# Kernel optimization log

Measured on AMD Instinct MI355X. Metric: run time of the kernel, lower is better.

## Reference

```python
import jax, jax.numpy as jnp
import numpy as np

MARGIN = 0.2
N_CLASSES = 100
BETA_INIT = 1.2
EPS = 1e-8


def setup_inputs() -> dict:
    key = jax.random.key(0)
    k1, k2, k3 = jax.random.split(key, 3)
    BS, DIM, T = 4096, 128, 500000
    batch = jax.random.normal(k1, (BS, DIM), dtype=jnp.float32)
    labels = jax.random.randint(k2, (BS,), 0, N_CLASSES, dtype=jnp.int64)
    triplets = jax.random.randint(k3, (T, 3), 0, BS, dtype=jnp.int64)
    beta = jnp.ones((N_CLASSES,), dtype=jnp.float32) * BETA_INIT
    return {"batch": batch, "labels": labels, "triplets": triplets, "beta": beta}


def reference(batch, labels, triplets, beta):
    # Gather anchor/positive/negative embedding rows: [T, DIM]
    a = batch[triplets[:, 0]]
    p = batch[triplets[:, 1]]
    n = batch[triplets[:, 2]]
    # Euclidean distances with the module's 1e-8 stabilizer: [T]
    d_ap = jnp.sqrt(jnp.sum((a - p) ** 2, axis=-1) + EPS)
    d_an = jnp.sqrt(jnp.sum((a - n) ** 2, axis=-1) + EPS)
    # Learned per-class beta, indexed by the anchor's label: [T]
    b = beta[labels[triplets[:, 0]]]
    pos_loss = jax.nn.relu(d_ap - b + MARGIN)
    neg_loss = jax.nn.relu(b - d_an + MARGIN)
    pair_count = (jnp.sum((pos_loss > 0.0).astype(jnp.float32))
                  + jnp.sum((neg_loss > 0.0).astype(jnp.float32)))
    total = jnp.sum(pos_loss + neg_loss)
    # If no active pairs, torch code returns the (zero) unnormalized sum.
    return jnp.where(pair_count > 0.0, total / jnp.maximum(pair_count, 1.0), total)
```

## Files before the change

### kernel.cpp

```cpp
#include <hip/hip_runtime.h>

#define MARGIN 0.2f
#define EPS 1e-8f
#define GRID_BLOCKS 2048

__global__ __launch_bounds__(256) void triplet_loss_kernel(
    const float* __restrict__ batch,
    const int* __restrict__ labels,
    const int* __restrict__ triplets,
    const float* __restrict__ beta,
    float* __restrict__ partial,
    int T)
{
    const int lane = threadIdx.x & 63;
    const int wid  = threadIdx.x >> 6;
    const int sub  = lane >> 3;
    const int fi   = lane & 7;

    float loss = 0.f, cnt = 0.f;

    for (int base = blockIdx.x * 32; base < T; base += gridDim.x * 32) {
        int t = base + wid * 8 + sub;
        if (t < T) {
            int ai = triplets[3 * t + 0];
            int pi = triplets[3 * t + 1];
            int ni = triplets[3 * t + 2];
            float b = beta[labels[ai]];
            const float4* __restrict__ arow = (const float4*)(batch + ((size_t)ai << 7));
            const float4* __restrict__ prow = (const float4*)(batch + ((size_t)pi << 7));
            const float4* __restrict__ nrow = (const float4*)(batch + ((size_t)ni << 7));
            float sap = 0.f, san = 0.f;
            #pragma unroll
            for (int k = 0; k < 4; ++k) {
                float4 av = arow[fi + 8 * k];
                float4 pv = prow[fi + 8 * k];
                float4 nv = nrow[fi + 8 * k];
                float d;
                d = av.x - pv.x; sap += d * d;
                d = av.y - pv.y; sap += d * d;
                d = av.z - pv.z; sap += d * d;
                d = av.w - pv.w; sap += d * d;
                d = av.x - nv.x; san += d * d;
                d = av.y - nv.y; san += d * d;
                d = av.z - nv.z; san += d * d;
                d = av.w - nv.w; san += d * d;
            }
            #pragma unroll
            for (int off = 4; off >= 1; off >>= 1) {
                sap += __shfl_xor(sap, off);
                san += __shfl_xor(san, off);
            }
            float d_ap = sqrtf(sap + EPS);
            float d_an = sqrtf(san + EPS);
            float pos = fmaxf(d_ap - b + MARGIN, 0.f);
            float neg = fmaxf(b - d_an + MARGIN, 0.f);
            loss += pos + neg;
            cnt  += (pos > 0.f ? 1.f : 0.f) + (neg > 0.f ? 1.f : 0.f);
        }
    }

    #pragma unroll
    for (int off = 32; off >= 1; off >>= 1) {
        loss += __shfl_down(loss, off);
        cnt  += __shfl_down(cnt, off);
    }
    __shared__ float sl[4], sc[4];
    if (lane == 0) { sl[wid] = loss; sc[wid] = cnt; }
    __syncthreads();
    if (threadIdx.x == 0) {
        partial[blockIdx.x * 2 + 0] = sl[0] + sl[1] + sl[2] + sl[3];
        partial[blockIdx.x * 2 + 1] = sc[0] + sc[1] + sc[2] + sc[3];
    }
}

__global__ __launch_bounds__(1024) void triplet_finalize_kernel(
    const float* __restrict__ partial, float* __restrict__ out, int nblocks)
{
    float L = 0.f, C = 0.f;
    for (int i = threadIdx.x; i < nblocks; i += blockDim.x) {
        L += partial[2 * i + 0];
        C += partial[2 * i + 1];
    }
    #pragma unroll
    for (int off = 32; off >= 1; off >>= 1) {
        L += __shfl_down(L, off);
        C += __shfl_down(C, off);
    }
    __shared__ float sl[16], sc[16];
    int wid  = threadIdx.x >> 6;
    int lane = threadIdx.x & 63;
    int nw   = blockDim.x >> 6;
    if (lane == 0) { sl[wid] = L; sc[wid] = C; }
    __syncthreads();
    if (threadIdx.x == 0) {
        float Lt = 0.f, Ct = 0.f;
        for (int i = 0; i < nw; ++i) { Lt += sl[i]; Ct += sc[i]; }
        Lt *= 0.125f;
        Ct *= 0.125f;
        out[0] = (Ct > 0.f) ? (Lt / fmaxf(Ct, 1.f)) : Lt;
    }
}

extern "C" void kernel_launch(void* const* d_in, const int* in_sizes, int n_in,
                              void* d_out, int out_size, void* d_ws, size_t ws_size,
                              hipStream_t stream) {
    const float* batch    = (const float*)d_in[0];
    const int*   labels   = (const int*)d_in[1];
    const int*   triplets = (const int*)d_in[2];
    const float* beta     = (const float*)d_in[3];
    float* out     = (float*)d_out;
    float* partial = (float*)d_ws;

    int T = in_sizes[2] / 3;
    int grid = GRID_BLOCKS;
    int groups = (T + 31) / 32;
    if (grid > groups) grid = groups;

    triplet_loss_kernel<<<grid, 256, 0, stream>>>(batch, labels, triplets, beta, partial, T);
    triplet_finalize_kernel<<<1, 1024, 0, stream>>>(partial, out, grid);
}
```

Measured before the change: 37.42 us.

## Convert embeddings to fp16 and compute distances with packed fdot2

Adds a pre-pass that converts the batch embeddings to fp16 in the workspace, then gathers fp16 rows (half the bytes per triplet) and accumulates squared differences with packed fdot2 into fp32. Each triplet is now handled by 4 lanes instead of 8, so a block covers 64 triplets per step, and the finalize scale is adjusted to match. The intent is to cut gather traffic and ALU work. The cost is an extra conversion launch and reduced precision on the differences, which could shift results near the relu thresholds.

```diff
diff --git a/kernel.cpp b/kernel.cpp
--- a/kernel.cpp
+++ b/kernel.cpp
@@ -4,7 +4,95 @@
 #define EPS 1e-8f
 #define GRID_BLOCKS 2048
 
-__global__ __launch_bounds__(256) void triplet_loss_kernel(
+typedef _Float16 h2 __attribute__((ext_vector_type(2)));
+typedef _Float16 h8 __attribute__((ext_vector_type(8)));
+union H8 { h8 v; h2 p[4]; };
+
+
+__global__ __launch_bounds__(256) void convert_f32_to_f16_kernel(
+    const float* __restrict__ in, _Float16* __restrict__ out, int n4)
+{
+    int i = blockIdx.x * blockDim.x + threadIdx.x;
+    if (i < n4) {
+        float4 f = *(const float4*)(in + 4 * (size_t)i);
+        h2 lo, hi;
+        lo.x = (_Float16)f.x; lo.y = (_Float16)f.y;
+        hi.x = (_Float16)f.z; hi.y = (_Float16)f.w;
+        *(h2*)(out + 4 * (size_t)i)     = lo;
+        *(h2*)(out + 4 * (size_t)i + 2) = hi;
+    }
+}
+
+__global__ __launch_bounds__(256) void triplet_loss_f16_kernel(
+    const _Float16* __restrict__ batch16,
+    const int* __restrict__ labels,
+    const int* __restrict__ triplets,
+    const float* __restrict__ beta,
+    float* __restrict__ partial,
+    int T)
+{
+    const int lane = threadIdx.x & 63;
+    const int wid  = threadIdx.x >> 6;
+    const int sub  = lane >> 2;
+    const int fi   = lane & 3;
+
+    float loss = 0.f, cnt = 0.f;
+
+    for (int base = blockIdx.x * 64; base < T; base += gridDim.x * 64) {
+        int t = base + wid * 16 + sub;
+        if (t < T) {
+            int ai = triplets[3 * t + 0];
+            int pi = triplets[3 * t + 1];
+            int ni = triplets[3 * t + 2];
+            float b = beta[labels[ai]];
+            const h8* __restrict__ arow = (const h8*)(batch16 + ((size_t)ai << 7));
+            const h8* __restrict__ prow = (const h8*)(batch16 + ((size_t)pi << 7));
+            const h8* __restrict__ nrow = (const h8*)(batch16 + ((size_t)ni << 7));
+            float sap = 0.f, san = 0.f;
+            #pragma unroll
+            for (int k = 0; k < 4; ++k) {
+                H8 a, p, n, dp, dn;
+                a.v = arow[fi + 4 * k];
+                p.v = prow[fi + 4 * k];
+                n.v = nrow[fi + 4 * k];
+                dp.v = a.v - p.v;
+                dn.v = a.v - n.v;
+                #pragma unroll
+                for (int j = 0; j < 4; ++j) {
+                    sap = __builtin_amdgcn_fdot2(dp.p[j], dp.p[j], sap, false);
+                    san = __builtin_amdgcn_fdot2(dn.p[j], dn.p[j], san, false);
+                }
+            }
+            #pragma unroll
+            for (int off = 2; off >= 1; off >>= 1) {
+                sap += __shfl_xor(sap, off);
+                san += __shfl_xor(san, off);
+            }
+            float d_ap = sqrtf(sap + EPS);
+            float d_an = sqrtf(san + EPS);
+            float pos = fmaxf(d_ap - b + MARGIN, 0.f);
+            float neg = fmaxf(b - d_an + MARGIN, 0.f);
+            loss += pos + neg;
+            cnt  += (pos > 0.f ? 1.f : 0.f) + (neg > 0.f ? 1.f : 0.f);
+        }
+    }
+
+    #pragma unroll
+    for (int off = 32; off >= 1; off >>= 1) {
+        loss += __shfl_down(loss, off);
+        cnt  += __shfl_down(cnt, off);
+    }
+    __shared__ float sl[4], sc[4];
+    if (lane == 0) { sl[wid] = loss; sc[wid] = cnt; }
+    __syncthreads();
+    if (threadIdx.x == 0) {
+        partial[blockIdx.x * 2 + 0] = sl[0] + sl[1] + sl[2] + sl[3];
+        partial[blockIdx.x * 2 + 1] = sc[0] + sc[1] + sc[2] + sc[3];
+    }
+}
+
+
+__global__ __launch_bounds__(256) void triplet_loss_f32_kernel(
     const float* __restrict__ batch,
     const int* __restrict__ labels,
     const int* __restrict__ triplets,
@@ -73,8 +161,10 @@
     }
 }
 
+
 __global__ __launch_bounds__(1024) void triplet_finalize_kernel(
-    const float* __restrict__ partial, float* __restrict__ out, int nblocks)
+    const float* __restrict__ partial, float* __restrict__ out, int nblocks,
+    float scale)
 {
     float L = 0.f, C = 0.f;
     for (int i = threadIdx.x; i < nblocks; i += blockDim.x) {
@@ -95,8 +185,8 @@
     if (threadIdx.x == 0) {
         float Lt = 0.f, Ct = 0.f;
         for (int i = 0; i < nw; ++i) { Lt += sl[i]; Ct += sc[i]; }
-        Lt *= 0.125f;
-        Ct *= 0.125f;
+        Lt *= scale;
+        Ct *= scale;
         out[0] = (Ct > 0.f) ? (Lt / fmaxf(Ct, 1.f)) : Lt;
     }
 }
@@ -108,14 +198,32 @@
     const int*   labels   = (const int*)d_in[1];
     const int*   triplets = (const int*)d_in[2];
     const float* beta     = (const float*)d_in[3];
-    float* out     = (float*)d_out;
-    float* partial = (float*)d_ws;
-
+    float* out = (float*)d_out;
+
+    int nbatch = in_sizes[0];
     int T = in_sizes[2] / 3;
-    int grid = GRID_BLOCKS;
-    int groups = (T + 31) / 32;
-    if (grid > groups) grid = groups;
-
-    triplet_loss_kernel<<<grid, 256, 0, stream>>>(batch, labels, triplets, beta, partial, T);
-    triplet_finalize_kernel<<<1, 1024, 0, stream>>>(partial, out, grid);
-}
+
+    size_t f16_bytes = (size_t)nbatch * sizeof(_Float16);
+    size_t need = f16_bytes + (size_t)GRID_BLOCKS * 2 * sizeof(float);
+
+    if (ws_size >= need) {
+        _Float16* batch16 = (_Float16*)d_ws;
+        float* partial = (float*)((char*)d_ws + f16_bytes);
+
+        int n4 = nbatch / 4;
+        convert_f32_to_f16_kernel<<<(n4 + 255) / 256, 256, 0, stream>>>(batch, batch16, n4);
+
+        int grid = GRID_BLOCKS;
+        int groups = (T + 63) / 64;
+        if (grid > groups) grid = groups;
+        triplet_loss_f16_kernel<<<grid, 256, 0, stream>>>(batch16, labels, triplets, beta, partial, T);
+        triplet_finalize_kernel<<<1, 1024, 0, stream>>>(partial, out, grid, 0.25f);
+    } else {
+        float* partial = (float*)d_ws;
+        int grid = GRID_BLOCKS;
+        int groups = (T + 31) / 32;
+        if (grid > groups) grid = groups;
+        triplet_loss_f32_kernel<<<grid, 256, 0, stream>>>(batch, labels, triplets, beta, partial, T);
+        triplet_finalize_kernel<<<1, 1024, 0, stream>>>(partial, out, grid, 0.125f);
+    }
+}
```

Result: faster. 30.97 us (-17.2%).

## Replace per-triplet row gathers with bf16 MFMA Gram matrix lookup

Applied to the files above, without the earlier changes.

Distances are rewritten as ||a||^2+||b||^2-2a·b. The new path precomputes row norms and a full 4096x4096 Gram matrix with bf16 MFMA, stored as fp16. Each triplet then does two scalar lookups into that matrix instead of gathering three 512-byte rows, which removes most of the per-triplet gather traffic. The cost is writing and randomly reading a 32MB matrix, extra launches, and reduced precision from bf16 inputs, fp16 storage and cancellation in the norm expansion. An fp32 fallback runs if the workspace is too small.

```diff
diff --git a/kernel.cpp b/kernel.cpp
--- a/kernel.cpp
+++ b/kernel.cpp
@@ -1,10 +1,171 @@
 #include <hip/hip_runtime.h>
+#include <hip/hip_fp16.h>
 
 #define MARGIN 0.2f
 #define EPS 1e-8f
-#define GRID_BLOCKS 2048
-
-__global__ __launch_bounds__(256) void triplet_loss_kernel(
+
+typedef short bf16x8 __attribute__((ext_vector_type(8)));
+typedef float f32x4 __attribute__((ext_vector_type(4)));
+
+static __device__ __forceinline__ unsigned short f32_to_bf16(float x) {
+    unsigned v = __float_as_uint(x);
+    unsigned r = (v + 0x7FFFu + ((v >> 16) & 1u)) >> 16;
+    return (unsigned short)r;
+}
+
+__global__ __launch_bounds__(256) void prep_norms_kernel(
+    const float* __restrict__ batch,
+    unsigned short* __restrict__ xb,
+    float* __restrict__ norms,
+    int rows)
+{
+    int gid = blockIdx.x * blockDim.x + threadIdx.x;
+    int r = gid >> 4, c = (gid & 15) * 8;
+    if (r >= rows) return;
+    const float4* src = (const float4*)(batch + (size_t)r * 128 + c);
+    float4 f0 = src[0], f1 = src[1];
+    float s = f0.x*f0.x + f0.y*f0.y + f0.z*f0.z + f0.w*f0.w
+            + f1.x*f1.x + f1.y*f1.y + f1.z*f1.z + f1.w*f1.w;
+    ushort4 u0, u1;
+    u0.x = f32_to_bf16(f0.x); u0.y = f32_to_bf16(f0.y);
+    u0.z = f32_to_bf16(f0.z); u0.w = f32_to_bf16(f0.w);
+    u1.x = f32_to_bf16(f1.x); u1.y = f32_to_bf16(f1.y);
+    u1.z = f32_to_bf16(f1.z); u1.w = f32_to_bf16(f1.w);
+    *(ushort4*)(xb + (size_t)r * 128 + c)     = u0;
+    *(ushort4*)(xb + (size_t)r * 128 + c + 4) = u1;
+    #pragma unroll
+    for (int off = 8; off >= 1; off >>= 1) s += __shfl_xor(s, off);
+    if ((gid & 15) == 0) norms[r] = s;
+}
+
+__global__ __launch_bounds__(256) void gram_kernel(
+    const unsigned short* __restrict__ xb,
+    __half* __restrict__ G,
+    int N)
+{
+    __shared__ unsigned short Atile[128][136];
+    __shared__ unsigned short Btile[128][136];
+
+    int nt = N >> 7;
+    int bi = blockIdx.x / nt, bj = blockIdx.x % nt;
+    int tid = threadIdx.x;
+
+    #pragma unroll
+    for (int pass = 0; pass < 8; ++pass) {
+        int r = pass * 16 + (tid >> 4);
+        int c = (tid & 15) * 8;
+        uint4 av = *(const uint4*)(xb + (size_t)(bi * 128 + r) * 128 + c);
+        uint4 bv = *(const uint4*)(xb + (size_t)(bj * 128 + r) * 128 + c);
+        *(uint4*)(&Atile[r][c]) = av;
+        *(uint4*)(&Btile[r][c]) = bv;
+    }
+    __syncthreads();
+
+    int w    = tid >> 6;
+    int lane = tid & 63;
+    int wr = (w >> 1) * 64, wc = (w & 1) * 64;
+    int fr = lane & 15, fg = lane >> 4;
+
+    f32x4 acc[4][4] = {};
+    #pragma unroll
+    for (int ks = 0; ks < 4; ++ks) {
+        bf16x8 af[4], bfv[4];
+        #pragma unroll
+        for (int fm = 0; fm < 4; ++fm)
+            af[fm] = *(const bf16x8*)(&Atile[wr + fm * 16 + fr][ks * 32 + fg * 8]);
+        #pragma unroll
+        for (int fn = 0; fn < 4; ++fn)
+            bfv[fn] = *(const bf16x8*)(&Btile[wc + fn * 16 + fr][ks * 32 + fg * 8]);
+        #pragma unroll
+        for (int fm = 0; fm < 4; ++fm)
+            #pragma unroll
+            for (int fn = 0; fn < 4; ++fn)
+                acc[fm][fn] = __builtin_amdgcn_mfma_f32_16x16x32_bf16(
+                    af[fm], bfv[fn], acc[fm][fn], 0, 0, 0);
+    }
+
+    int rowbase = bi * 128 + wr, colbase = bj * 128 + wc;
+    #pragma unroll
+    for (int fm = 0; fm < 4; ++fm)
+        #pragma unroll
+        for (int fn = 0; fn < 4; ++fn)
+            #pragma unroll
+            for (int i = 0; i < 4; ++i) {
+                int row = rowbase + fm * 16 + fg * 4 + i;
+                int col = colbase + fn * 16 + fr;
+                G[(size_t)row * N + col] = __float2half(acc[fm][fn][i]);
+            }
+}
+
+__global__ __launch_bounds__(256) void triplet_kernel(
+    const __half* __restrict__ G,
+    const float* __restrict__ norms,
+    const int* __restrict__ labels,
+    const int* __restrict__ triplets,
+    const float* __restrict__ beta,
+    float* __restrict__ partial,
+    int T, int N)
+{
+    int t = blockIdx.x * blockDim.x + threadIdx.x;
+    float loss = 0.f, cnt = 0.f;
+    if (t < T) {
+        int a = triplets[3 * t + 0];
+        int p = triplets[3 * t + 1];
+        int n = triplets[3 * t + 2];
+        float b  = beta[labels[a]];
+        float na = norms[a], npv = norms[p], nn = norms[n];
+        float gap = __half2float(G[(size_t)a * N + p]);
+        float gan = __half2float(G[(size_t)a * N + n]);
+        float dap = sqrtf(fmaxf(na + npv - 2.f * gap, 0.f) + EPS);
+        float dan = sqrtf(fmaxf(na + nn  - 2.f * gan, 0.f) + EPS);
+        float pos = fmaxf(dap - b + MARGIN, 0.f);
+        float neg = fmaxf(b - dan + MARGIN, 0.f);
+        loss = pos + neg;
+        cnt  = (pos > 0.f ? 1.f : 0.f) + (neg > 0.f ? 1.f : 0.f);
+    }
+    #pragma unroll
+    for (int off = 32; off >= 1; off >>= 1) {
+        loss += __shfl_down(loss, off);
+        cnt  += __shfl_down(cnt, off);
+    }
+    __shared__ float sl[4], sc[4];
+    int wid = threadIdx.x >> 6, lane = threadIdx.x & 63;
+    if (lane == 0) { sl[wid] = loss; sc[wid] = cnt; }
+    __syncthreads();
+    if (threadIdx.x == 0) {
+        partial[blockIdx.x * 2 + 0] = sl[0] + sl[1] + sl[2] + sl[3];
+        partial[blockIdx.x * 2 + 1] = sc[0] + sc[1] + sc[2] + sc[3];
+    }
+}
+
+__global__ __launch_bounds__(1024) void triplet_finalize_kernel(
+    const float* __restrict__ partial, float* __restrict__ out, int nblocks,
+    float scale)
+{
+    float L = 0.f, C = 0.f;
+    for (int i = threadIdx.x; i < nblocks; i += blockDim.x) {
+        L += partial[2 * i + 0];
+        C += partial[2 * i + 1];
+    }
+    #pragma unroll
+    for (int off = 32; off >= 1; off >>= 1) {
+        L += __shfl_down(L, off);
+        C += __shfl_down(C, off);
+    }
+    __shared__ float sl[16], sc[16];
+    int wid = threadIdx.x >> 6, lane = threadIdx.x & 63;
+    int nw = blockDim.x >> 6;
+    if (lane == 0) { sl[wid] = L; sc[wid] = C; }
+    __syncthreads();
+    if (threadIdx.x == 0) {
+        float Lt = 0.f, Ct = 0.f;
+        for (int i = 0; i < nw; ++i) { Lt += sl[i]; Ct += sc[i]; }
+        Lt *= scale; Ct *= scale;
+        out[0] = (Ct > 0.f) ? (Lt / fmaxf(Ct, 1.f)) : Lt;
+    }
+}
+
+__global__ __launch_bounds__(256) void triplet_loss_f32_kernel(
     const float* __restrict__ batch,
     const int* __restrict__ labels,
     const int* __restrict__ triplets,
@@ -16,9 +177,7 @@
     const int wid  = threadIdx.x >> 6;
     const int sub  = lane >> 3;
     const int fi   = lane & 7;
-
     float loss = 0.f, cnt = 0.f;
-
     for (int base = blockIdx.x * 32; base < T; base += gridDim.x * 32) {
         int t = base + wid * 8 + sub;
         if (t < T) {
@@ -58,7 +217,6 @@
             cnt  += (pos > 0.f ? 1.f : 0.f) + (neg > 0.f ? 1.f : 0.f);
         }
     }
-
     #pragma unroll
     for (int off = 32; off >= 1; off >>= 1) {
         loss += __shfl_down(loss, off);
@@ -70,34 +228,6 @@
     if (threadIdx.x == 0) {
         partial[blockIdx.x * 2 + 0] = sl[0] + sl[1] + sl[2] + sl[3];
         partial[blockIdx.x * 2 + 1] = sc[0] + sc[1] + sc[2] + sc[3];
-    }
-}
-
-__global__ __launch_bounds__(1024) void triplet_finalize_kernel(
-    const float* __restrict__ partial, float* __restrict__ out, int nblocks)
-{
-    float L = 0.f, C = 0.f;
-    for (int i = threadIdx.x; i < nblocks; i += blockDim.x) {
-        L += partial[2 * i + 0];
-        C += partial[2 * i + 1];
-    }
-    #pragma unroll
-    for (int off = 32; off >= 1; off >>= 1) {
-        L += __shfl_down(L, off);
-        C += __shfl_down(C, off);
-    }
-    __shared__ float sl[16], sc[16];
-    int wid  = threadIdx.x >> 6;
-    int lane = threadIdx.x & 63;
-    int nw   = blockDim.x >> 6;
-    if (lane == 0) { sl[wid] = L; sc[wid] = C; }
-    __syncthreads();
-    if (threadIdx.x == 0) {
-        float Lt = 0.f, Ct = 0.f;
-        for (int i = 0; i < nw; ++i) { Lt += sl[i]; Ct += sc[i]; }
-        Lt *= 0.125f;
-        Ct *= 0.125f;
-        out[0] = (Ct > 0.f) ? (Lt / fmaxf(Ct, 1.f)) : Lt;
     }
 }
 
@@ -108,14 +238,44 @@
     const int*   labels   = (const int*)d_in[1];
     const int*   triplets = (const int*)d_in[2];
     const float* beta     = (const float*)d_in[3];
-    float* out     = (float*)d_out;
-    float* partial = (float*)d_ws;
-
-    int T = in_sizes[2] / 3;
-    int grid = GRID_BLOCKS;
-    int groups = (T + 31) / 32;
-    if (grid > groups) grid = groups;
-
-    triplet_loss_kernel<<<grid, 256, 0, stream>>>(batch, labels, triplets, beta, partial, T);
-    triplet_finalize_kernel<<<1, 1024, 0, stream>>>(partial, out, grid);
-}
+    float* out = (float*)d_out;
+
+    int nbatch = in_sizes[0];
+    int rows   = nbatch / 128;
+    int T      = in_sizes[2] / 3;
+
+    size_t xb_bytes    = ((size_t)nbatch * 2 + 255) & ~(size_t)255;
+    size_t norms_bytes = ((size_t)rows * 4 + 255) & ~(size_t)255;
+    size_t G_bytes     = ((size_t)rows * rows * 2 + 255) & ~(size_t)255;
+    int tblocks = (T + 255) / 256;
+    size_t part_bytes  = (size_t)tblocks * 2 * sizeof(float);
+    size_t need = xb_bytes + norms_bytes + G_bytes + part_bytes;
+
+    bool ok = (rows % 128 == 0) && (nbatch % 128 == 0) && (ws_size >= need);
+
+    if (ok) {
+        unsigned short* xb = (unsigned short*)d_ws;
+        float* norms       = (float*)((char*)d_ws + xb_bytes);
+        __half* G          = (__half*)((char*)d_ws + xb_bytes + norms_bytes);
+        float* partial     = (float*)((char*)d_ws + xb_bytes + norms_bytes + G_bytes);
+
+        int k1_threads = rows * 16;
+        prep_norms_kernel<<<(k1_threads + 255) / 256, 256, 0, stream>>>(
+            batch, xb, norms, rows);
+
+        int nt = rows / 128;
+        gram_kernel<<<nt * nt, 256, 0, stream>>>(xb, G, rows);
+
+        triplet_kernel<<<tblocks, 256, 0, stream>>>(
+            G, norms, labels, triplets, beta, partial, T, rows);
+
+        triplet_finalize_kernel<<<1, 1024, 0, stream>>>(partial, out, tblocks, 1.0f);
+    } else {
+        float* partial = (float*)d_ws;
+        int grid = 2048;
+        int groups = (T + 31) / 32;
+        if (grid > groups) grid = groups;
+        triplet_loss_f32_kernel<<<grid, 256, 0, stream>>>(batch, labels, triplets, beta, partial, T);
+        triplet_finalize_kernel<<<1, 1024, 0, stream>>>(partial, out, grid, 0.125f);
+    }
+}
```

Result: slower. 44.73 us (+19.5%).
